# Kernel optimization log

Measured on AMD Instinct MI355X. Metric: run time of the kernel, lower is better.

Reference implementation:

```python
import jax, jax.numpy as jnp
import numpy as np

# ---- config (mirrors conf dict passed to RegionLoss.__init__) ----
ANCHORS = jnp.array([[1.3221, 1.73145], [3.19275, 4.00944], [5.05587, 8.09892],
                     [9.47112, 4.84053], [11.2364, 10.0071]], dtype=jnp.float32)
NUM_CLASSES = 80
OBJECT_SCALE = 5.0
NO_OBJECT_SCALE = 1.0
CLASS_SCALE = 1.0
COORD_SCALE = 1.0
SIL_THRESH = 0.6
SEEN = 0  # fresh module -> seen < 12800 warm-start branch is active


def _iou_center(a, b):
    """IoU of center-format boxes (cx, cy, w, h); a, b broadcastable [..., 4]."""
    ax1, ax2 = a[..., 0] - a[..., 2] * 0.5, a[..., 0] + a[..., 2] * 0.5
    ay1, ay2 = a[..., 1] - a[..., 3] * 0.5, a[..., 1] + a[..., 3] * 0.5
    bx1, bx2 = b[..., 0] - b[..., 2] * 0.5, b[..., 0] + b[..., 2] * 0.5
    by1, by2 = b[..., 1] - b[..., 3] * 0.5, b[..., 1] + b[..., 3] * 0.5
    iw = jnp.maximum(jnp.minimum(ax2, bx2) - jnp.maximum(ax1, bx1), 0.0)
    ih = jnp.maximum(jnp.minimum(ay2, by2) - jnp.maximum(ay1, by1), 0.0)
    inter = iw * ih
    union = a[..., 2] * a[..., 3] + b[..., 2] * b[..., 3] - inter
    return inter / union


def setup_inputs() -> dict:
    key = jax.random.key(0)
    k1, k2, k3, k4 = jax.random.split(key, 4)
    B, A, C, H, W, NBOX = 32, 5, NUM_CLASSES, 52, 52, 50
    pred = jax.random.normal(k1, (B, A * (C + 5), H, W), dtype=jnp.float32)
    cls = jax.random.randint(k2, (B, NBOX, 1), 0, C).astype(jnp.float32)
    xy = jax.random.uniform(k3, (B, NBOX, 2), minval=0.02, maxval=0.98, dtype=jnp.float32)
    wh = jax.random.uniform(k4, (B, NBOX, 2), minval=0.05, maxval=0.4, dtype=jnp.float32)
    target = jnp.concatenate([cls, xy, wh], axis=-1)  # (B, NBOX, 5): cls,x,y,w,h in [0,1]
    return {"pred": pred, "target": target, "train_out": 0}


def _region_loss(pred, target):
    B, H, W = pred.shape[0], pred.shape[2], pred.shape[3]
    A, C = ANCHORS.shape[0], NUM_CLASSES
    nbox = target.shape[1]
    p = pred.reshape(B, A, C + 5, H, W)

    txy = jax.nn.sigmoid(p[:, :, 0:2])                 # (B,A,2,H,W)
    twh = p[:, :, 2:4]                                 # (B,A,2,H,W)
    pred_no_off = jnp.concatenate([txy, twh], axis=2)  # (B,A,4,H,W)
    pred_conf = jax.nn.sigmoid(p[:, :, 4])             # (B,A,H,W)
    cls_logits = p[:, :, 5:]                           # (B,A,C,H,W)

    # decode boxes to grid units (detached in the original)
    grid_x = jnp.arange(W, dtype=p.dtype)              # broadcasts along W (last dim)
    grid_y = jnp.arange(H, dtype=p.dtype)[:, None]     # broadcasts along H
    aw = ANCHORS[:, 0][None, :, None, None]
    ah = ANCHORS[:, 1][None, :, None, None]
    bx = txy[:, :, 0] + grid_x
    by = txy[:, :, 1] + grid_y
    bw = jnp.exp(twh[:, :, 0]) * aw
    bh = jnp.exp(twh[:, :, 1]) * ah
    pred_boxes = jax.lax.stop_gradient(jnp.stack([bx, by, bw, bh], axis=-1))  # (B,A,H,W,4)

    # ground truth in grid units
    scale = jnp.array([W, H, W, H], dtype=p.dtype)
    gt = target[:, :, 1:5] * scale                     # (B,nbox,4) center format
    valid = target[:, :, 1] > 0                        # sentinel: x == 0 terminates

    # conf mask: zero-out cells whose best IoU vs any GT exceeds sil_thresh
    pb_flat = pred_boxes.reshape(B, A * H * W, 4)
    ious = _iou_center(gt[:, :, None, :], pb_flat[:, None, :, :])  # (B,nbox,A*H*W)
    ious = jnp.where(valid[:, :, None], ious, 0.0)
    max_iou = jnp.max(ious, axis=1).reshape(B, A, H, W)
    conf_mask = jnp.where(max_iou > SIL_THRESH, 0.0, NO_OBJECT_SCALE)

    # best anchor per GT via width/height-only IoU (boxes at origin)
    gw, gh = gt[..., 2], gt[..., 3]
    inter = jnp.minimum(gw[..., None], ANCHORS[:, 0]) * jnp.minimum(gh[..., None], ANCHORS[:, 1])
    union = gw[..., None] * gh[..., None] + ANCHORS[:, 0] * ANCHORS[:, 1] - inter
    best_a = jnp.argmax(inter / union, axis=-1)        # (B,nbox)

    gi = jnp.clip(gt[..., 0].astype(jnp.int32), 0, W - 1)
    gj = jnp.clip(gt[..., 1].astype(jnp.int32), 0, H - 1)
    b_idx = jnp.broadcast_to(jnp.arange(B)[:, None], (B, nbox))
    bi = jnp.where(valid, b_idx, B)                    # invalid GTs -> OOB batch, dropped

    aw_b = ANCHORS[best_a, 0]
    ah_b = ANCHORS[best_a, 1]
    tx_t = gt[..., 0] - gi.astype(p.dtype)
    ty_t = gt[..., 1] - gj.astype(p.dtype)
    tw_t = jnp.log(gw / aw_b)
    th_t = jnp.log(gh / ah_b)

    pred_box_at = pred_boxes[b_idx, best_a, gj, gi]    # (B,nbox,4) decoded box at GT cell
    iou_gt = _iou_center(gt, pred_box_at)              # (B,nbox)

    # initialize targets/masks (seen < 12800 warm start)
    if SEEN < 12800:
        coord_mask = jnp.ones((B, A, H, W), dtype=p.dtype)
        target_box = jnp.zeros((B, A, 4, H, W), dtype=p.dtype).at[:, :, 0:2].set(0.5)
    else:
        coord_mask = jnp.zeros((B, A, H, W), dtype=p.dtype)
        target_box = jnp.zeros((B, A, 4, H, W), dtype=p.dtype)
    cls_mask = jnp.zeros((B, A, H, W), dtype=p.dtype)
    target_conf = jnp.zeros((B, A, H, W), dtype=p.dtype)
    target_cls = jnp.zeros((B, A, H, W), dtype=p.dtype)

    coord_mask = coord_mask.at[bi, best_a, gj, gi].set(1.0, mode='drop')
    cls_mask = cls_mask.at[bi, best_a, gj, gi].set(1.0, mode='drop')
    conf_mask = conf_mask.at[bi, best_a, gj, gi].set(OBJECT_SCALE, mode='drop')
    target_box = target_box.at[bi, best_a, 0, gj, gi].set(tx_t, mode='drop')
    target_box = target_box.at[bi, best_a, 1, gj, gi].set(ty_t, mode='drop')
    target_box = target_box.at[bi, best_a, 2, gj, gi].set(tw_t, mode='drop')
    target_box = target_box.at[bi, best_a, 3, gj, gi].set(th_t, mode='drop')
    target_conf = target_conf.at[bi, best_a, gj, gi].set(iou_gt, mode='drop')
    target_cls = target_cls.at[bi, best_a, gj, gi].set(target[:, :, 0], mode='drop')

    # losses
    half = jnp.asarray(0.5, p.dtype)
    loss_x = COORD_SCALE * jnp.sum(((pred_no_off[:, :, 0] - target_box[:, :, 0]) * coord_mask) ** 2) * half
    loss_y = COORD_SCALE * jnp.sum(((pred_no_off[:, :, 1] - target_box[:, :, 1]) * coord_mask) ** 2) * half
    loss_w = COORD_SCALE * jnp.sum(((pred_no_off[:, :, 2] - target_box[:, :, 2]) * coord_mask) ** 2) * half
    loss_h = COORD_SCALE * jnp.sum(((pred_no_off[:, :, 3] - target_box[:, :, 3]) * coord_mask) ** 2) * half
    loss_conf = jnp.sum(((pred_conf - target_conf) * jnp.sqrt(conf_mask)) ** 2) * half

    logp = jax.nn.log_softmax(cls_logits, axis=2)      # (B,A,C,H,W)
    tcls = jnp.clip(target_cls.astype(jnp.int32), 0, C - 1)
    ce = -jnp.take_along_axis(logp, tcls[:, :, None], axis=2)[:, :, 0]  # (B,A,H,W)
    loss_cls = CLASS_SCALE * jnp.sum(cls_mask * ce)

    loss = loss_x + loss_y + loss_w + loss_h + loss_conf + loss_cls
    return loss, loss_x, loss_y, loss_w, loss_h, loss_conf, loss_cls


def reference(pred, target, train_out):
    out = _region_loss(pred, target)
    if train_out:
        return out
    return out[0]
```

## Files before the change

### kernel.cpp

```cpp
#include <hip/hip_runtime.h>
#include <math.h>

#define BB 32
#define AA 5
#define CC 80
#define HH 52
#define WW 52
#define NBOX 50
#define HWSZ (HH*WW)
#define CELLS (AA*HWSZ)
#define NF 16

__constant__ float d_aw[AA] = {1.3221f, 3.19275f, 5.05587f, 9.47112f, 11.2364f};
__constant__ float d_ah[AA] = {1.73145f, 4.00944f, 8.09892f, 4.84053f, 10.0071f};

__device__ __forceinline__ float sigmoidf(float x) { return 1.f / (1.f + __expf(-x) * 0.f + expf(-x) - expf(-x) + expf(-x)); }

__device__ __forceinline__ float sig(float x) { return 1.f / (1.f + expf(-x)); }

__global__ void region_prep(const float* __restrict__ pred,
                            const float* __restrict__ target,
                            float* __restrict__ boxws) {
    int b = blockIdx.x;
    int j = threadIdx.x;
    if (j >= NBOX) return;
    const float* t = target + ((size_t)b * NBOX + j) * 5;
    float cls = t[0];
    float raw_x = t[1];
    float gx = t[1] * (float)WW;
    float gy = t[2] * (float)HH;
    float gw = t[3] * (float)WW;
    float gh = t[4] * (float)HH;
    float valid = (raw_x > 0.f) ? 1.f : 0.f;

    int best = 0; float bestv = -1.f;
    for (int a = 0; a < AA; ++a) {
        float inter = fminf(gw, d_aw[a]) * fminf(gh, d_ah[a]);
        float uni = gw * gh + d_aw[a] * d_ah[a] - inter;
        float r = inter / uni;
        if (r > bestv) { bestv = r; best = a; }
    }
    int gi = (int)gx; gi = gi < 0 ? 0 : (gi > WW - 1 ? WW - 1 : gi);
    int gj = (int)gy; gj = gj < 0 ? 0 : (gj > HH - 1 ? HH - 1 : gj);
    float tx_t = gx - (float)gi;
    float ty_t = gy - (float)gj;
    float tw_t = logf(gw / d_aw[best]);
    float th_t = logf(gh / d_ah[best]);

    size_t base = ((size_t)(b * AA + best) * (CC + 5)) * HWSZ + (size_t)gj * WW + gi;
    float p0 = pred[base];
    float p1 = pred[base + HWSZ];
    float p2 = pred[base + 2 * HWSZ];
    float p3 = pred[base + 3 * HWSZ];
    float px = sig(p0) + (float)gi;
    float py = sig(p1) + (float)gj;
    float pw = expf(p2) * d_aw[best];
    float ph = expf(p3) * d_ah[best];

    float ax1 = gx - gw * 0.5f, ax2 = gx + gw * 0.5f;
    float ay1 = gy - gh * 0.5f, ay2 = gy + gh * 0.5f;
    float bx1 = px - pw * 0.5f, bx2 = px + pw * 0.5f;
    float by1 = py - ph * 0.5f, by2 = py + ph * 0.5f;
    float iw = fmaxf(fminf(ax2, bx2) - fmaxf(ax1, bx1), 0.f);
    float ih = fmaxf(fminf(ay2, by2) - fmaxf(ay1, by1), 0.f);
    float inter = iw * ih;
    float iou_gt = inter / (gw * gh + pw * ph - inter);

    float* o = boxws + ((size_t)b * NBOX + j) * NF;
    o[0] = valid;
    o[1] = (float)best;
    o[2] = (float)gi;
    o[3] = (float)gj;
    o[4] = tx_t; o[5] = ty_t; o[6] = tw_t; o[7] = th_t;
    o[8] = iou_gt;
    o[9] = cls;
    o[10] = ax1; o[11] = ax2; o[12] = ay1; o[13] = ay2;
    o[14] = gw * gh;
    o[15] = 0.f;
}

__global__ __launch_bounds__(256) void region_loss(const float* __restrict__ pred,
                                                   const float* __restrict__ boxws,
                                                   float* __restrict__ out) {
    __shared__ float sh[NBOX * NF];
    __shared__ float wsum[4];
    int b = blockIdx.y;
    int tid = threadIdx.x;
    for (int i = tid; i < NBOX * NF; i += 256)
        sh[i] = boxws[(size_t)b * NBOX * NF + i];
    __syncthreads();

    int c = blockIdx.x * 256 + tid;
    float lsum = 0.f;
    if (c < CELLS) {
        int a = c / HWSZ;
        int rem = c - a * HWSZ;
        int hh = rem / WW;
        int wwi = rem - hh * WW;
        size_t base = ((size_t)(b * AA + a) * (CC + 5)) * HWSZ + rem;
        float p0 = pred[base];
        float p1 = pred[base + HWSZ];
        float p2 = pred[base + 2 * HWSZ];
        float p3 = pred[base + 3 * HWSZ];
        float p4 = pred[base + 4 * HWSZ];
        float tx = sig(p0);
        float ty = sig(p1);
        float conf = sig(p4);
        float bx = tx + (float)wwi;
        float by = ty + (float)hh;
        float bw = expf(p2) * d_aw[a];
        float bh = expf(p3) * d_ah[a];
        float px1 = bx - bw * 0.5f, px2 = bx + bw * 0.5f;
        float py1 = by - bh * 0.5f, py2 = by + bh * 0.5f;
        float parea = bw * bh;

        float maxiou = 0.f;
        int win = -1;
        #pragma unroll 5
        for (int j = 0; j < NBOX; ++j) {
            const float* s = sh + j * NF;
            if (s[0] != 0.f) {
                float iw = fmaxf(fminf(px2, s[11]) - fmaxf(px1, s[10]), 0.f);
                float ih = fmaxf(fminf(py2, s[13]) - fmaxf(py1, s[12]), 0.f);
                float inter = iw * ih;
                float iou = inter / (parea + s[14] - inter);
                maxiou = fmaxf(maxiou, iou);
                if ((int)s[1] == a && (int)s[2] == wwi && (int)s[3] == hh) win = j;
            }
        }

        float dx, dy, dw, dh, lconf;
        if (win >= 0) {
            const float* s = sh + win * NF;
            dx = tx - s[4]; dy = ty - s[5]; dw = p2 - s[6]; dh = p3 - s[7];
            float d = conf - s[8];
            lconf = 2.5f * d * d;
            int tcls = (int)s[9];
            tcls = tcls < 0 ? 0 : (tcls > CC - 1 ? CC - 1 : tcls);
            size_t cbase = base + 5 * (size_t)HWSZ;
            float m = -INFINITY, ssum = 0.f, vt = 0.f;
            for (int k = 0; k < CC; ++k) {
                float v = pred[cbase + (size_t)k * HWSZ];
                if (k == tcls) vt = v;
                if (v > m) { ssum = ssum * expf(m - v) + 1.f; m = v; }
                else       { ssum += expf(v - m); }
            }
            lsum += (m + logf(ssum)) - vt;
        } else {
            dx = tx - 0.5f; dy = ty - 0.5f; dw = p2; dh = p3;
            float cm = (maxiou > 0.6f) ? 0.f : 1.f;
            lconf = 0.5f * cm * conf * conf;
        }
        lsum += 0.5f * (dx * dx + dy * dy + dw * dw + dh * dh) + lconf;
    }

    for (int off = 32; off > 0; off >>= 1)
        lsum += __shfl_down(lsum, off, 64);
    int wave = tid >> 6;
    if ((tid & 63) == 0) wsum[wave] = lsum;
    __syncthreads();
    if (tid == 0) {
        float tot = wsum[0] + wsum[1] + wsum[2] + wsum[3];
        atomicAdd(out, tot);
    }
}

extern "C" void kernel_launch(void* const* d_in, const int* in_sizes, int n_in,
                              void* d_out, int out_size, void* d_ws, size_t ws_size,
                              hipStream_t stream) {
    const float* pred = (const float*)d_in[0];
    const float* target = (const float*)d_in[1];
    float* out = (float*)d_out;
    float* boxws = (float*)d_ws;

    hipMemsetAsync(out, 0, sizeof(float) * out_size, stream);
    region_prep<<<dim3(BB), dim3(64), 0, stream>>>(pred, target, boxws);
    dim3 grid((CELLS + 255) / 256, BB);
    region_loss<<<grid, dim3(256), 0, stream>>>(pred, boxws, out);
}
```

Before: 249.2 us.

## Move per-object class cross-entropy into a separate wave-parallel kernel

Pulls the 80-class log-softmax for matched cells out of the per-cell loss kernel into a new kernel. In that kernel one wave handles one target box, reading classes across lanes and reducing with shuffles. The prep kernel now packs box data as float4 records and marks whether each box is the last writer for its cell, so duplicates are counted once. The main loop loses its valid-check branch (invalid boxes are encoded so they never match and give zero IoU) and reads float4 from shared memory. The aim is to remove the serial 80-load tail that stalled divergent threads in the main kernel, at the cost of one extra kernel launch and an O(NBOX^2) duplicate check in prep.

```diff
diff --git a/kernel.cpp b/kernel.cpp
--- a/kernel.cpp
+++ b/kernel.cpp
@@ -9,53 +9,55 @@
 #define NBOX 50
 #define HWSZ (HH*WW)
 #define CELLS (AA*HWSZ)
-#define NF 16
 
 __constant__ float d_aw[AA] = {1.3221f, 3.19275f, 5.05587f, 9.47112f, 11.2364f};
 __constant__ float d_ah[AA] = {1.73145f, 4.00944f, 8.09892f, 4.84053f, 10.0071f};
 
-__device__ __forceinline__ float sigmoidf(float x) { return 1.f / (1.f + __expf(-x) * 0.f + expf(-x) - expf(-x) + expf(-x)); }
-
 __device__ __forceinline__ float sig(float x) { return 1.f / (1.f + expf(-x)); }
 
-__global__ void region_prep(const float* __restrict__ pred,
-                            const float* __restrict__ target,
-                            float* __restrict__ boxws) {
-    int b = blockIdx.x;
-    int j = threadIdx.x;
-    if (j >= NBOX) return;
-    const float* t = target + ((size_t)b * NBOX + j) * 5;
-    float cls = t[0];
-    float raw_x = t[1];
+
+__device__ __forceinline__ void cell_of(const float* t, int& best, int& gi, int& gj, float& valid) {
     float gx = t[1] * (float)WW;
     float gy = t[2] * (float)HH;
     float gw = t[3] * (float)WW;
     float gh = t[4] * (float)HH;
-    float valid = (raw_x > 0.f) ? 1.f : 0.f;
-
-    int best = 0; float bestv = -1.f;
+    valid = (t[1] > 0.f) ? 1.f : 0.f;
+    best = 0; float bestv = -1.f;
+    #pragma unroll
     for (int a = 0; a < AA; ++a) {
         float inter = fminf(gw, d_aw[a]) * fminf(gh, d_ah[a]);
         float uni = gw * gh + d_aw[a] * d_ah[a] - inter;
         float r = inter / uni;
         if (r > bestv) { bestv = r; best = a; }
     }
-    int gi = (int)gx; gi = gi < 0 ? 0 : (gi > WW - 1 ? WW - 1 : gi);
-    int gj = (int)gy; gj = gj < 0 ? 0 : (gj > HH - 1 ? HH - 1 : gj);
+    gi = (int)gx; gi = gi < 0 ? 0 : (gi > WW - 1 ? WW - 1 : gi);
+    gj = (int)gy; gj = gj < 0 ? 0 : (gj > HH - 1 ? HH - 1 : gj);
+}
+
+__global__ void region_prep(const float* __restrict__ pred,
+                            const float* __restrict__ target,
+                            float4* __restrict__ boxws) {
+    int b = blockIdx.x;
+    int j = threadIdx.x;
+    if (j >= NBOX) return;
+    const float* t = target + ((size_t)b * NBOX + j) * 5;
+    float gx = t[1] * (float)WW;
+    float gy = t[2] * (float)HH;
+    float gw = t[3] * (float)WW;
+    float gh = t[4] * (float)HH;
+    int best, gi, gj; float valid;
+    cell_of(t, best, gi, gj, valid);
+
     float tx_t = gx - (float)gi;
     float ty_t = gy - (float)gj;
     float tw_t = logf(gw / d_aw[best]);
     float th_t = logf(gh / d_ah[best]);
 
     size_t base = ((size_t)(b * AA + best) * (CC + 5)) * HWSZ + (size_t)gj * WW + gi;
-    float p0 = pred[base];
-    float p1 = pred[base + HWSZ];
-    float p2 = pred[base + 2 * HWSZ];
-    float p3 = pred[base + 3 * HWSZ];
-    float px = sig(p0) + (float)gi;
-    float py = sig(p1) + (float)gj;
-    float pw = expf(p2) * d_aw[best];
-    float ph = expf(p3) * d_ah[best];
+    float px = sig(pred[base]) + (float)gi;
+    float py = sig(pred[base + HWSZ]) + (float)gj;
+    float pw = expf(pred[base + 2 * HWSZ]) * d_aw[best];
+    float ph = expf(pred[base + 3 * HWSZ]) * d_ah[best];
 
     float ax1 = gx - gw * 0.5f, ax2 = gx + gw * 0.5f;
     float ay1 = gy - gh * 0.5f, ay2 = gy + gh * 0.5f;
@@ -66,28 +68,73 @@
     float inter = iw * ih;
     float iou_gt = inter / (gw * gh + pw * ph - inter);
 
-    float* o = boxws + ((size_t)b * NBOX + j) * NF;
-    o[0] = valid;
-    o[1] = (float)best;
-    o[2] = (float)gi;
-    o[3] = (float)gj;
-    o[4] = tx_t; o[5] = ty_t; o[6] = tw_t; o[7] = th_t;
-    o[8] = iou_gt;
-    o[9] = cls;
-    o[10] = ax1; o[11] = ax2; o[12] = ay1; o[13] = ay2;
-    o[14] = gw * gh;
-    o[15] = 0.f;
+    float is_last = 1.f;
+    for (int j2 = j + 1; j2 < NBOX; ++j2) {
+        const float* t2 = target + ((size_t)b * NBOX + j2) * 5;
+        int b2, i2, jj2; float v2;
+        cell_of(t2, b2, i2, jj2, v2);
+        if (v2 != 0.f && b2 == best && i2 == gi && jj2 == gj) is_last = 0.f;
+    }
+
+    float4* o = boxws + ((size_t)b * NBOX + j) * 4;
+    if (valid != 0.f) {
+        o[0] = make_float4(ax1, ax2, ay1, ay2);
+        o[1] = make_float4(gw * gh, (float)best, (float)gi, (float)gj);
+    } else {
+        o[0] = make_float4(0.f, 0.f, 0.f, 0.f);
+        o[1] = make_float4(0.f, -1.f, -1.f, -1.f);
+    }
+    o[2] = make_float4(tx_t, ty_t, tw_t, th_t);
+    o[3] = make_float4(iou_gt, t[0], valid, is_last);
+}
+
+__device__ __forceinline__ float wave_max(float v) {
+    #pragma unroll
+    for (int off = 32; off > 0; off >>= 1) v = fmaxf(v, __shfl_xor(v, off, 64));
+    return v;
+}
+__device__ __forceinline__ float wave_sum(float v) {
+    #pragma unroll
+    for (int off = 32; off > 0; off >>= 1) v += __shfl_xor(v, off, 64);
+    return v;
+}
+
+__global__ __launch_bounds__(256) void region_ce(const float* __restrict__ pred,
+                                                 const float4* __restrict__ boxws,
+                                                 float* __restrict__ out) {
+    int b = blockIdx.x;
+    int wave = threadIdx.x >> 6;
+    int lane = threadIdx.x & 63;
+    float acc = 0.f;
+    for (int j = wave; j < NBOX; j += 4) {
+        const float4* r = boxws + ((size_t)b * NBOX + j) * 4;
+        float4 r1 = r[1];
+        float4 r3 = r[3];
+        if (r3.z == 0.f || r3.w == 0.f) continue;
+        int a = (int)r1.y, gi = (int)r1.z, gj = (int)r1.w;
+        size_t cbase = ((size_t)(b * AA + a) * (CC + 5) + 5) * HWSZ + (size_t)gj * WW + gi;
+        float v1 = pred[cbase + (size_t)lane * HWSZ];
+        float v2 = (lane < CC - 64) ? pred[cbase + (size_t)(lane + 64) * HWSZ] : -INFINITY;
+        float mx = wave_max(fmaxf(v1, v2));
+        float s = expf(v1 - mx) + ((lane < CC - 64) ? expf(v2 - mx) : 0.f);
+        s = wave_sum(s);
+        int tcls = (int)r3.y;
+        tcls = tcls < 0 ? 0 : (tcls > CC - 1 ? CC - 1 : tcls);
+        float vt = ((lane == tcls) ? v1 : 0.f) + ((lane + 64 == tcls) ? v2 : 0.f);
+        vt = wave_sum(vt);
+        if (lane == 0) acc += (mx + logf(s)) - vt;
+    }
+    if (lane == 0 && acc != 0.f) atomicAdd(out, acc);
 }
 
 __global__ __launch_bounds__(256) void region_loss(const float* __restrict__ pred,
-                                                   const float* __restrict__ boxws,
+                                                   const float4* __restrict__ boxws,
                                                    float* __restrict__ out) {
-    __shared__ float sh[NBOX * NF];
+    __shared__ float4 sh[NBOX * 4];
     __shared__ float wsum[4];
     int b = blockIdx.y;
     int tid = threadIdx.x;
-    for (int i = tid; i < NBOX * NF; i += 256)
-        sh[i] = boxws[(size_t)b * NBOX * NF + i];
+    if (tid < NBOX * 4) sh[tid] = boxws[(size_t)b * NBOX * 4 + tid];
     __syncthreads();
 
     int c = blockIdx.x * 256 + tid;
@@ -113,55 +160,46 @@
         float px1 = bx - bw * 0.5f, px2 = bx + bw * 0.5f;
         float py1 = by - bh * 0.5f, py2 = by + bh * 0.5f;
         float parea = bw * bh;
+        float af = (float)a, wf = (float)wwi, hf = (float)hh;
 
         float maxiou = 0.f;
         int win = -1;
-        #pragma unroll 5
+        #pragma unroll 2
         for (int j = 0; j < NBOX; ++j) {
-            const float* s = sh + j * NF;
-            if (s[0] != 0.f) {
-                float iw = fmaxf(fminf(px2, s[11]) - fmaxf(px1, s[10]), 0.f);
-                float ih = fmaxf(fminf(py2, s[13]) - fmaxf(py1, s[12]), 0.f);
-                float inter = iw * ih;
-                float iou = inter / (parea + s[14] - inter);
-                maxiou = fmaxf(maxiou, iou);
-                if ((int)s[1] == a && (int)s[2] == wwi && (int)s[3] == hh) win = j;
-            }
+            float4 r0 = sh[j * 4 + 0];
+            float4 r1 = sh[j * 4 + 1];
+            float iw = fmaxf(fminf(px2, r0.y) - fmaxf(px1, r0.x), 0.f);
+            float ih = fmaxf(fminf(py2, r0.w) - fmaxf(py1, r0.z), 0.f);
+            float inter = iw * ih;
+            float iou = inter / (parea + r1.x - inter);
+            maxiou = fmaxf(maxiou, iou);
+            bool m = (r1.y == af) & (r1.z == wf) & (r1.w == hf);
+            win = m ? j : win;
         }
 
         float dx, dy, dw, dh, lconf;
         if (win >= 0) {
-            const float* s = sh + win * NF;
-            dx = tx - s[4]; dy = ty - s[5]; dw = p2 - s[6]; dh = p3 - s[7];
-            float d = conf - s[8];
+            float4 r2 = sh[win * 4 + 2];
+            float4 r3 = sh[win * 4 + 3];
+            dx = tx - r2.x; dy = ty - r2.y; dw = p2 - r2.z; dh = p3 - r2.w;
+            float d = conf - r3.x;
             lconf = 2.5f * d * d;
-            int tcls = (int)s[9];
-            tcls = tcls < 0 ? 0 : (tcls > CC - 1 ? CC - 1 : tcls);
-            size_t cbase = base + 5 * (size_t)HWSZ;
-            float m = -INFINITY, ssum = 0.f, vt = 0.f;
-            for (int k = 0; k < CC; ++k) {
-                float v = pred[cbase + (size_t)k * HWSZ];
-                if (k == tcls) vt = v;
-                if (v > m) { ssum = ssum * expf(m - v) + 1.f; m = v; }
-                else       { ssum += expf(v - m); }
-            }
-            lsum += (m + logf(ssum)) - vt;
         } else {
             dx = tx - 0.5f; dy = ty - 0.5f; dw = p2; dh = p3;
             float cm = (maxiou > 0.6f) ? 0.f : 1.f;
             lconf = 0.5f * cm * conf * conf;
         }
-        lsum += 0.5f * (dx * dx + dy * dy + dw * dw + dh * dh) + lconf;
-    }
-
+        lsum = 0.5f * (dx * dx + dy * dy + dw * dw + dh * dh) + lconf;
+    }
+
+    #pragma unroll
     for (int off = 32; off > 0; off >>= 1)
         lsum += __shfl_down(lsum, off, 64);
     int wave = tid >> 6;
     if ((tid & 63) == 0) wsum[wave] = lsum;
     __syncthreads();
     if (tid == 0) {
-        float tot = wsum[0] + wsum[1] + wsum[2] + wsum[3];
-        atomicAdd(out, tot);
+        atomicAdd(out, wsum[0] + wsum[1] + wsum[2] + wsum[3]);
     }
 }
 
@@ -171,10 +209,11 @@
     const float* pred = (const float*)d_in[0];
     const float* target = (const float*)d_in[1];
     float* out = (float*)d_out;
-    float* boxws = (float*)d_ws;
+    float4* boxws = (float4*)d_ws;
 
     hipMemsetAsync(out, 0, sizeof(float) * out_size, stream);
     region_prep<<<dim3(BB), dim3(64), 0, stream>>>(pred, target, boxws);
+    region_ce<<<dim3(BB), dim3(256), 0, stream>>>(pred, boxws, out);
     dim3 grid((CELLS + 255) / 256, BB);
     region_loss<<<grid, dim3(256), 0, stream>>>(pred, boxws, out);
 }
```

Measured after the change: 249.1 us. No clear change (-0.1%).
